# Kernel tuning notes

Measured on AMD Instinct MI355X. Metric: run time of the kernel, lower is better.

## Reference

```python
import jax, jax.numpy as jnp
import numpy as np

IN_F = 8192
OUT_F = 8192
MAX_STATES = 100
THRESHOLD = MAX_STATES // 2  # 50
TARGET_FIRING_RATE = 0.1


def setup_inputs() -> dict:
    key = jax.random.key(0)
    k0, k1 = jax.random.split(key)
    spike_input = jax.random.uniform(k0, (IN_F,), dtype=jnp.float32)
    # buffer init: randint(threshold-5, threshold+5) -> values in [45, 55)
    synapse_states = jax.random.randint(k1, (OUT_F, IN_F), THRESHOLD - 5, THRESHOLD + 5).astype(jnp.float32)
    membrane_potential = jnp.zeros((OUT_F,), dtype=jnp.float32)
    adaptive_threshold = jnp.full((OUT_F,), 2.0, dtype=jnp.float32)
    eligibility_trace = jnp.zeros((OUT_F, IN_F), dtype=jnp.float32)
    return {
        "spike_input": spike_input,
        "synapse_states": synapse_states,
        "membrane_potential": membrane_potential,
        "adaptive_threshold": adaptive_threshold,
        "eligibility_trace": eligibility_trace,
    }


def reference(spike_input, synapse_states, membrane_potential, adaptive_threshold, eligibility_trace):
    # ternary (0/1) weights from state threshold
    w = (synapse_states > THRESHOLD).astype(jnp.float32)  # [out, in]
    x = jnp.clip(spike_input * 2.0, 0.0, 1.0)             # [in]
    current = jnp.einsum('oi,i->o', w, x)                 # [out]
    v_mem = membrane_potential * 0.7 + current            # decayed membrane + input current
    spikes = (v_mem >= adaptive_threshold).astype(jnp.float32)
    new_threshold = jnp.clip(adaptive_threshold + (spikes - TARGET_FIRING_RATE) * 0.05, 0.5, 5.0)
    new_trace = jnp.clip(eligibility_trace * 0.8 + jnp.outer(spikes, x), 0.0, 3.0)
    new_v_mem = v_mem * (1.0 - spikes) * 0.3              # reset fired neurons, leak rest
    return spikes, new_v_mem, new_threshold, new_trace
```

## Files before the change

### kernel.cpp

```cpp
#include <hip/hip_runtime.h>

#define IN_F 8192
#define OUT_F 8192
#define THRESHOLD_F 50.0f
#define TARGET_RATE 0.1f

__global__ __launch_bounds__(256) void snn_reduce_kernel(
    const float* __restrict__ spike_input,
    const float* __restrict__ synapse_states,
    const float* __restrict__ membrane_potential,
    const float* __restrict__ adaptive_threshold,
    float* __restrict__ out_spikes,
    float* __restrict__ out_vmem,
    float* __restrict__ out_thresh)
{
    __shared__ float wave_sum[4];

    const int o   = blockIdx.x;
    const int tid = threadIdx.x;

    const float4* s4 = (const float4*)(synapse_states + (size_t)o * IN_F);
    const float4* x4 = (const float4*)spike_input;

    float sum = 0.0f;
    #pragma unroll
    for (int k = 0; k < 8; ++k) {
        int idx = tid + k * 256;
        float4 s = s4[idx];
        float4 v = x4[idx];
        v.x = fminf(fmaxf(v.x * 2.0f, 0.0f), 1.0f);
        v.y = fminf(fmaxf(v.y * 2.0f, 0.0f), 1.0f);
        v.z = fminf(fmaxf(v.z * 2.0f, 0.0f), 1.0f);
        v.w = fminf(fmaxf(v.w * 2.0f, 0.0f), 1.0f);
        sum += (s.x > THRESHOLD_F ? v.x : 0.0f)
             + (s.y > THRESHOLD_F ? v.y : 0.0f)
             + (s.z > THRESHOLD_F ? v.z : 0.0f)
             + (s.w > THRESHOLD_F ? v.w : 0.0f);
    }
    #pragma unroll
    for (int off = 32; off > 0; off >>= 1)
        sum += __shfl_down(sum, off, 64);
    if ((tid & 63) == 0) wave_sum[tid >> 6] = sum;
    __syncthreads();

    if (tid == 0) {
        float current = wave_sum[0] + wave_sum[1] + wave_sum[2] + wave_sum[3];
        float v_mem = membrane_potential[o] * 0.7f + current;
        float thr   = adaptive_threshold[o];
        float spike = (v_mem >= thr) ? 1.0f : 0.0f;
        out_spikes[o] = spike;
        out_vmem[o]   = v_mem * (1.0f - spike) * 0.3f;
        out_thresh[o] = fminf(fmaxf(thr + (spike - TARGET_RATE) * 0.05f, 0.5f), 5.0f);
    }
}

__global__ __launch_bounds__(256) void snn_trace_kernel(
    const float* __restrict__ spike_input,
    const float* __restrict__ eligibility_trace,
    const float* __restrict__ out_spikes,
    float* __restrict__ out_trace)
{
    const int total4 = (OUT_F * IN_F) / 4;
    const int nthreads = gridDim.x * blockDim.x;
    const float4* e4 = (const float4*)eligibility_trace;
    const float4* x4 = (const float4*)spike_input;
    float4* t4 = (float4*)out_trace;

    for (int idx = blockIdx.x * blockDim.x + threadIdx.x; idx < total4; idx += nthreads) {
        int row = idx >> 11;
        int col = idx & 2047;
        float  spike = out_spikes[row];
        float4 e = e4[idx];
        float4 v = x4[col];
        float4 t;
        t.x = fminf(fmaxf(e.x * 0.8f + spike * fminf(fmaxf(v.x * 2.0f, 0.0f), 1.0f), 0.0f), 3.0f);
        t.y = fminf(fmaxf(e.y * 0.8f + spike * fminf(fmaxf(v.y * 2.0f, 0.0f), 1.0f), 0.0f), 3.0f);
        t.z = fminf(fmaxf(e.z * 0.8f + spike * fminf(fmaxf(v.z * 2.0f, 0.0f), 1.0f), 0.0f), 3.0f);
        t.w = fminf(fmaxf(e.w * 0.8f + spike * fminf(fmaxf(v.w * 2.0f, 0.0f), 1.0f), 0.0f), 3.0f);
        t4[idx] = t;
    }
}

extern "C" void kernel_launch(void* const* d_in, const int* in_sizes, int n_in,
                              void* d_out, int out_size, void* d_ws, size_t ws_size,
                              hipStream_t stream) {
    const float* spike_input        = (const float*)d_in[0];
    const float* synapse_states     = (const float*)d_in[1];
    const float* membrane_potential = (const float*)d_in[2];
    const float* adaptive_threshold = (const float*)d_in[3];
    const float* eligibility_trace  = (const float*)d_in[4];

    float* out = (float*)d_out;
    float* out_spikes = out;
    float* out_vmem   = out + OUT_F;
    float* out_thresh = out + 2 * OUT_F;
    float* out_trace  = out + 3 * OUT_F;

    snn_reduce_kernel<<<OUT_F, 256, 0, stream>>>(
        spike_input, synapse_states, membrane_potential, adaptive_threshold,
        out_spikes, out_vmem, out_thresh);

    snn_trace_kernel<<<8192, 256, 0, stream>>>(
        spike_input, eligibility_trace, out_spikes, out_trace);
}
```

Before: 582.3 us.

## Fuse reduction and trace update into one wave-per-row kernel with nontemporal accesses

```diff
diff --git a/kernel.cpp b/kernel.cpp
--- a/kernel.cpp
+++ b/kernel.cpp
@@ -5,29 +5,31 @@
 #define THRESHOLD_F 50.0f
 #define TARGET_RATE 0.1f
 
-__global__ __launch_bounds__(256) void snn_reduce_kernel(
+typedef float f32x4 __attribute__((ext_vector_type(4)));
+
+__global__ __launch_bounds__(256) void snn_wave_fused(
     const float* __restrict__ spike_input,
     const float* __restrict__ synapse_states,
     const float* __restrict__ membrane_potential,
     const float* __restrict__ adaptive_threshold,
+    const float* __restrict__ eligibility_trace,
     float* __restrict__ out_spikes,
     float* __restrict__ out_vmem,
-    float* __restrict__ out_thresh)
+    float* __restrict__ out_thresh,
+    float* __restrict__ out_trace)
 {
-    __shared__ float wave_sum[4];
+    const int row  = (blockIdx.x << 2) + (threadIdx.x >> 6);
+    const int lane = threadIdx.x & 63;
 
-    const int o   = blockIdx.x;
-    const int tid = threadIdx.x;
-
-    const float4* s4 = (const float4*)(synapse_states + (size_t)o * IN_F);
-    const float4* x4 = (const float4*)spike_input;
+    const f32x4* x4 = (const f32x4*)spike_input;
+    const f32x4* s4 = (const f32x4*)(synapse_states + (size_t)row * IN_F);
 
     float sum = 0.0f;
-    #pragma unroll
-    for (int k = 0; k < 8; ++k) {
-        int idx = tid + k * 256;
-        float4 s = s4[idx];
-        float4 v = x4[idx];
+    #pragma unroll 8
+    for (int k = 0; k < 32; ++k) {
+        int idx = lane + (k << 6);
+        f32x4 s = __builtin_nontemporal_load(&s4[idx]);
+        f32x4 v = x4[idx];
         v.x = fminf(fmaxf(v.x * 2.0f, 0.0f), 1.0f);
         v.y = fminf(fmaxf(v.y * 2.0f, 0.0f), 1.0f);
         v.z = fminf(fmaxf(v.z * 2.0f, 0.0f), 1.0f);
@@ -38,46 +40,31 @@
              + (s.w > THRESHOLD_F ? v.w : 0.0f);
     }
     #pragma unroll
-    for (int off = 32; off > 0; off >>= 1)
-        sum += __shfl_down(sum, off, 64);
-    if ((tid & 63) == 0) wave_sum[tid >> 6] = sum;
-    __syncthreads();
+    for (int m = 1; m < 64; m <<= 1)
+        sum += __shfl_xor(sum, m, 64);
 
-    if (tid == 0) {
-        float current = wave_sum[0] + wave_sum[1] + wave_sum[2] + wave_sum[3];
-        float v_mem = membrane_potential[o] * 0.7f + current;
-        float thr   = adaptive_threshold[o];
-        float spike = (v_mem >= thr) ? 1.0f : 0.0f;
-        out_spikes[o] = spike;
-        out_vmem[o]   = v_mem * (1.0f - spike) * 0.3f;
-        out_thresh[o] = fminf(fmaxf(thr + (spike - TARGET_RATE) * 0.05f, 0.5f), 5.0f);
+    float v_mem = membrane_potential[row] * 0.7f + sum;
+    float thr   = adaptive_threshold[row];
+    float spike = (v_mem >= thr) ? 1.0f : 0.0f;
+    if (lane == 0) {
+        out_spikes[row] = spike;
+        out_vmem[row]   = v_mem * (1.0f - spike) * 0.3f;
+        out_thresh[row] = fminf(fmaxf(thr + (spike - TARGET_RATE) * 0.05f, 0.5f), 5.0f);
     }
-}
 
-__global__ __launch_bounds__(256) void snn_trace_kernel(
-    const float* __restrict__ spike_input,
-    const float* __restrict__ eligibility_trace,
-    const float* __restrict__ out_spikes,
-    float* __restrict__ out_trace)
-{
-    const int total4 = (OUT_F * IN_F) / 4;
-    const int nthreads = gridDim.x * blockDim.x;
-    const float4* e4 = (const float4*)eligibility_trace;
-    const float4* x4 = (const float4*)spike_input;
-    float4* t4 = (float4*)out_trace;
-
-    for (int idx = blockIdx.x * blockDim.x + threadIdx.x; idx < total4; idx += nthreads) {
-        int row = idx >> 11;
-        int col = idx & 2047;
-        float  spike = out_spikes[row];
-        float4 e = e4[idx];
-        float4 v = x4[col];
-        float4 t;
+    const f32x4* e4 = (const f32x4*)(eligibility_trace + (size_t)row * IN_F);
+    f32x4* t4 = (f32x4*)(out_trace + (size_t)row * IN_F);
+    #pragma unroll 8
+    for (int k = 0; k < 32; ++k) {
+        int idx = lane + (k << 6);
+        f32x4 e = __builtin_nontemporal_load(&e4[idx]);
+        f32x4 v = x4[idx];
+        f32x4 t;
         t.x = fminf(fmaxf(e.x * 0.8f + spike * fminf(fmaxf(v.x * 2.0f, 0.0f), 1.0f), 0.0f), 3.0f);
         t.y = fminf(fmaxf(e.y * 0.8f + spike * fminf(fmaxf(v.y * 2.0f, 0.0f), 1.0f), 0.0f), 3.0f);
         t.z = fminf(fmaxf(e.z * 0.8f + spike * fminf(fmaxf(v.z * 2.0f, 0.0f), 1.0f), 0.0f), 3.0f);
         t.w = fminf(fmaxf(e.w * 0.8f + spike * fminf(fmaxf(v.w * 2.0f, 0.0f), 1.0f), 0.0f), 3.0f);
-        t4[idx] = t;
+        __builtin_nontemporal_store(t, &t4[idx]);
     }
 }
 
@@ -96,10 +83,7 @@
     float* out_thresh = out + 2 * OUT_F;
     float* out_trace  = out + 3 * OUT_F;
 
-    snn_reduce_kernel<<<OUT_F, 256, 0, stream>>>(
+    snn_wave_fused<<<OUT_F / 4, 256, 0, stream>>>(
         spike_input, synapse_states, membrane_potential, adaptive_threshold,
-        out_spikes, out_vmem, out_thresh);
-
-    snn_trace_kernel<<<8192, 256, 0, stream>>>(
-        spike_input, eligibility_trace, out_spikes, out_trace);
+        eligibility_trace, out_spikes, out_vmem, out_thresh, out_trace);
 }
```

Measured after the change: 579.3 us. About the same (-0.5%).
